# Kernel optimization log

Hardware: AMD Instinct MI355X
Metric: run time of the kernel (lower is better)

## Reference

```python
import jax, jax.numpy as jnp
import numpy as np
from jax import lax

B = 2
IMG = 640.0
MIN_LEVEL, MAX_LEVEL = 3, 7
NUM_CLASSES = 91          # includes background (index 0)
MAX_TOTAL = 100
IOU_THR = 0.3
SCORE_THR = 0.05
PRE_NMS = 5000
BBOX_CLIP = float(np.log(1000.0 / 16.0))  # standard box-transform clip


def _level_anchors(level):
    """RetinaNet-style anchors for one pyramid level, [H*W*9, 4] in (y1,x1,y2,x2)."""
    stride = 2 ** level
    feat = int(IMG) // stride
    cy = (np.arange(feat, dtype=np.float32) + 0.5) * stride
    cx = (np.arange(feat, dtype=np.float32) + 0.5) * stride
    cy, cx = np.meshgrid(cy, cx, indexing='ij')
    base = 4.0 * stride
    anchors = []
    for octave in (2 ** 0.0, 2 ** (1.0 / 3.0), 2 ** (2.0 / 3.0)):
        for ar in (0.5, 1.0, 2.0):
            h = base * octave * np.sqrt(ar)
            w = base * octave / np.sqrt(ar)
            anchors.append(np.stack([cy - h / 2, cx - w / 2, cy + h / 2, cx + w / 2], -1))
    a = np.stack(anchors, -2).reshape(-1, 4)
    return a.astype(np.float32)


def setup_inputs():
    key = jax.random.key(0)
    inp = {}
    for level in range(MIN_LEVEL, MAX_LEVEL + 1):
        anc = _level_anchors(level)
        n = anc.shape[0]
        key, kb, kc = jax.random.split(key, 3)
        inp[f'box_outputs_{level}'] = 0.2 * jax.random.normal(kb, (B, n, 4), jnp.float32)
        inp[f'class_outputs_{level}'] = jax.random.normal(kc, (B, n, NUM_CLASSES), jnp.float32) - 2.0
        inp[f'anchor_boxes_{level}'] = jnp.broadcast_to(jnp.asarray(anc)[None], (B, n, 4))
    inp['image_shape'] = jnp.full((B, 2), IMG, jnp.float32)
    return inp


def _decode_boxes(enc, anchors):
    # faithful to box_utils.decode_boxes (with the +1/-1 pixel convention)
    dy, dx = enc[..., 0], enc[..., 1]
    dh = jnp.minimum(enc[..., 2], BBOX_CLIP)
    dw = jnp.minimum(enc[..., 3], BBOX_CLIP)
    ah = anchors[..., 2] - anchors[..., 0] + 1.0
    aw = anchors[..., 3] - anchors[..., 1] + 1.0
    ayc = anchors[..., 0] + 0.5 * ah
    axc = anchors[..., 1] + 0.5 * aw
    yc = dy * ah + ayc
    xc = dx * aw + axc
    h = jnp.exp(dh) * ah
    w = jnp.exp(dw) * aw
    ymin = yc - 0.5 * h
    xmin = xc - 0.5 * w
    return jnp.stack([ymin, xmin, ymin + h - 1.0, xmin + w - 1.0], axis=-1)


def _clip_boxes(boxes, image_shape):
    h = image_shape[:, 0:1]
    w = image_shape[:, 1:2]
    max_len = jnp.stack([h, w, h, w], axis=-1)  # [B,1,4]
    return jnp.clip(boxes, 0.0, max_len)


def _greedy_nms(scores, boxes):
    """Sorted greedy NMS over one (batch, class) lane.
    scores: [K] sorted descending (filtered entries are -1), boxes: [K,4].
    Returns top MAX_TOTAL selected (score, box) in descending score order,
    padded with score=-1 / zero boxes (matches sorted_non_max_suppression_padded).
    """
    areas = (boxes[:, 2] - boxes[:, 0]) * (boxes[:, 3] - boxes[:, 1])

    def step(active, _):
        masked = jnp.where(active, scores, -jnp.inf)
        i = jnp.argmax(masked)
        s = masked[i]
        valid = s > -1.0
        b = boxes[i]
        yy1 = jnp.maximum(b[0], boxes[:, 0])
        xx1 = jnp.maximum(b[1], boxes[:, 1])
        yy2 = jnp.minimum(b[2], boxes[:, 2])
        xx2 = jnp.minimum(b[3], boxes[:, 3])
        inter = jnp.maximum(yy2 - yy1, 0.0) * jnp.maximum(xx2 - xx1, 0.0)
        iou = inter / ((b[2] - b[0]) * (b[3] - b[1]) + areas - inter + 1e-8)
        active = active & (iou <= IOU_THR)
        active = active.at[i].set(False)
        out_s = jnp.where(valid, s, -1.0)
        out_b = jnp.where(valid, b, jnp.zeros_like(b))
        return active, (out_s, out_b)

    _, (sel_s, sel_b) = lax.scan(step, jnp.ones(scores.shape[0], bool), None, length=MAX_TOTAL)
    return sel_s, sel_b


def reference(box_outputs_3, box_outputs_4, box_outputs_5, box_outputs_6, box_outputs_7,
              class_outputs_3, class_outputs_4, class_outputs_5, class_outputs_6, class_outputs_7,
              anchor_boxes_3, anchor_boxes_4, anchor_boxes_5, anchor_boxes_6, anchor_boxes_7,
              image_shape):
    box_list = [box_outputs_3, box_outputs_4, box_outputs_5, box_outputs_6, box_outputs_7]
    cls_list = [class_outputs_3, class_outputs_4, class_outputs_5, class_outputs_6, class_outputs_7]
    anc_list = [anchor_boxes_3, anchor_boxes_4, anchor_boxes_5, anchor_boxes_6, anchor_boxes_7]

    boxes, scores = [], []
    for bo, co, an in zip(box_list, cls_list, anc_list):
        scores.append(jax.nn.sigmoid(co)[..., 1:])            # drop background class 0
        boxes.append(_clip_boxes(_decode_boxes(bo, an), image_shape))
    boxes = jnp.concatenate(boxes, axis=1)                     # [B,N,4] class-agnostic
    scores = jnp.concatenate(scores, axis=1)                   # [B,N,C]

    scores_t = jnp.transpose(scores, (0, 2, 1))                # [B,C,N]
    k = min(scores_t.shape[-1], PRE_NMS)
    top_s, idx = lax.top_k(scores_t, k)                        # [B,C,K]
    top_b = jax.vmap(lambda b, i: b[i])(boxes, idx)            # [B,C,K,4]

    # filter_boxes_by_scores: score -> -1, boxes -> 0 below threshold
    mask = top_s >= SCORE_THR
    top_s = jnp.where(mask, top_s, -1.0)
    top_b = top_b * mask[..., None].astype(top_b.dtype)

    sel_s, sel_b = jax.vmap(jax.vmap(_greedy_nms))(top_s, top_b)  # [B,C,T], [B,C,T,4]
    Bsz, C, T = sel_s.shape
    classes = jnp.broadcast_to(jnp.arange(C, dtype=jnp.int32)[None, :, None], (Bsz, C, T))

    flat_s = sel_s.reshape(Bsz, C * T)
    flat_b = sel_b.reshape(Bsz, C * T, 4)
    flat_c = classes.reshape(Bsz, C * T)

    final_s, fidx = lax.top_k(flat_s, MAX_TOTAL)
    final_b = jnp.take_along_axis(flat_b, fidx[..., None], axis=1)
    final_c = jnp.take_along_axis(flat_c, fidx, axis=1) + 1    # nmsed_classes += 1
    valid = jnp.sum((final_s > -1.0).astype(jnp.int32), axis=1)
    return final_b, final_s, final_c, valid
```

## Files before the change

### kernel.cpp

```cpp
#include <hip/hip_runtime.h>
#include <hip/hip_bf16.h>

typedef unsigned long long u64;
typedef unsigned int u32;

#define A_TOTAL 76725
#define NCLS 90
#define KTOP 5000u
#define MAXT 100
#define KTHR 0x3D4CCCCDu
#define TCAP 2048u
#define SCAP 512u
#define BSTG 1024

__device__ __forceinline__ u64 pack_key(u32 k, u32 i) {
  return ((u64)k << 32) | (u64)(0xFFFFFFFFu - i);
}

__device__ __forceinline__ int dig05(u64 k) {
  float s = __uint_as_float((u32)(k >> 32));
  int d = (int)((s - 0.5f) * 8175.0f);
  return min(max(d, 0), 4095);
}

__device__ __forceinline__ void cut4096w(const u32* hh, u32 need, int wl,
                                         u32& B, u32& incl, u32& above, u32& total) {
  int lo = wl << 6;
  u32 s = 0;
  #pragma unroll
  for (int j = 0; j < 64; ++j) s += hh[lo + j];
  u32 suf = s;
  #pragma unroll
  for (int off = 1; off < 64; off <<= 1) {
    u32 v = __shfl_down(suf, off, 64);
    if (wl < 64 - off) suf += v;
  }
  total = __shfl(suf, 0, 64);
  if (total < need) { B = 0; incl = total; above = 0; return; }
  u32 sufnext = suf - s;
  bool cross = (suf >= need) && (sufnext < need);
  u64 bal = __ballot(cross);
  int gl = (int)__ffsll((unsigned long long)bal) - 1;
  int glo = gl << 6;
  u32 aboveG = __shfl(sufnext, gl, 64);
  u32 hb = hh[glo + wl];
  u32 sufb = hb;
  #pragma unroll
  for (int off = 1; off < 64; off <<= 1) {
    u32 v = __shfl_down(sufb, off, 64);
    if (wl < 64 - off) sufb += v;
  }
  bool c2 = (aboveG + sufb >= need) && (aboveG + sufb - hb < need);
  u64 bal2 = __ballot(c2);
  int jB = (int)__ffsll((unsigned long long)bal2) - 1;
  B = (u32)(glo + jB);
  incl = aboveG + __shfl(sufb, jB, 64);
  above = incl - __shfl(hb, jB, 64);
}

__device__ __forceinline__ void bitonic_desc(u64* a, u32 n, int tid, int nth) {
  u32 P = 2; while (P < n) P <<= 1;
  for (u32 i = tid; i < P; i += nth) if (i >= n) a[i] = 0ULL;
  __syncthreads();
  for (u32 kk = 2; kk <= P; kk <<= 1) {
    for (u32 jj = kk >> 1; jj; jj >>= 1) {
      for (u32 i = tid; i < P; i += nth) {
        u32 ixj = i ^ jj;
        if (ixj > i) {
          u64 x = a[i], y = a[ixj];
          bool up = ((i & kk) == 0);
          if (up ? (x < y) : (x > y)) { a[i] = y; a[ixj] = x; }
        }
      }
      __syncthreads();
    }
  }
}

__device__ __forceinline__ int lazy_scan_g(const u64* key_s, const float4* boxes4, size_t bbase,
                                           int C, float4* wbox, float* outS, float* outB,
                                           int w, int wl) {
  int cur = 0;
  while (w < MAXT && cur < C) {
    int p = cur + wl;
    bool alive = (p < C);
    u64 kk = alive ? key_s[p] : 0ull;
    float4 mybox = make_float4(0.f, 0.f, 0.f, 0.f);
    if (alive) {
      u32 idx = 0xFFFFFFFFu - (u32)(kk & 0xFFFFFFFFull);
      mybox = boxes4[bbase + idx];
    }
    float myarea = (mybox.z - mybox.x) * (mybox.w - mybox.y);
    for (int j = 0; j < w; ++j) {
      float4 pb = wbox[j];
      float yy1 = fmaxf(pb.x, mybox.x), xx1 = fmaxf(pb.y, mybox.y);
      float yy2 = fminf(pb.z, mybox.z), xx2 = fminf(pb.w, mybox.w);
      float inter = fmaxf(yy2 - yy1, 0.0f) * fmaxf(xx2 - xx1, 0.0f);
      bool bad = false;
      if (inter > 0.0f) {
        float pa = (pb.z - pb.x) * (pb.w - pb.y);
        bad = inter / (pa + myarea - inter + 1e-8f) > 0.3f;
      }
      alive = alive && !bad;
    }
    for (;;) {
      u64 bal = __ballot(alive);
      if (bal == 0ull) break;
      int js = (int)__ffsll((unsigned long long)bal) - 1;
      float4 pb;
      pb.x = __shfl(mybox.x, js, 64);
      pb.y = __shfl(mybox.y, js, 64);
      pb.z = __shfl(mybox.z, js, 64);
      pb.w = __shfl(mybox.w, js, 64);
      u64 wk = __shfl(kk, js, 64);
      if (wl == 0) {
        outS[w] = __uint_as_float((u32)(wk >> 32));
        *(float4*)(outB + w * 4) = pb;
        wbox[w] = pb;
      }
      w++;
      if (w >= MAXT) break;
      if (wl <= js) alive = false;
      else if (alive) {
        float yy1 = fmaxf(pb.x, mybox.x), xx1 = fmaxf(pb.y, mybox.y);
        float yy2 = fminf(pb.z, mybox.z), xx2 = fminf(pb.w, mybox.w);
        float inter = fmaxf(yy2 - yy1, 0.0f) * fmaxf(xx2 - xx1, 0.0f);
        if (inter > 0.0f) {
          float pa = (pb.z - pb.x) * (pb.w - pb.y);
          if (inter / (pa + myarea - inter + 1e-8f) > 0.3f) alive = false;
        }
      }
    }
    cur += 64;
  }
  return w;
}

__global__ __launch_bounds__(256) void zero_kernel(u32* __restrict__ p, int n) {
  int i = blockIdx.x * 256 + threadIdx.x;
  if (i < n) p[i] = 0;
}

__device__ __forceinline__ void coll_elem(int i, float x, int b, int base, int slice,
                                          u64* __restrict__ listT_g, u32* __restrict__ cnt_pad) {
  if (x >= 0.0f) {
    u32 a = (u32)i / 91u;
    u32 c = (u32)i - a * 91u;
    if (c != 0u) {
      float s = 1.0f / (1.0f + expf(-x));
      int lane = b * NCLS + (int)c - 1;
      u32 idx = (u32)base + a;
      u32 p = atomicAdd(&cnt_pad[lane * 128 + slice * 16], 1u);
      if (p < SCAP) listT_g[(((size_t)lane * 8 + slice) << 9) + p] = pack_key(__float_as_uint(s), idx);
    }
  }
}

__global__ __launch_bounds__(256) void front_kernel(
    const float* __restrict__ bx0, const float* __restrict__ bx1, const float* __restrict__ bx2,
    const float* __restrict__ bx3, const float* __restrict__ bx4,
    const float* __restrict__ an0, const float* __restrict__ an1, const float* __restrict__ an2,
    const float* __restrict__ an3, const float* __restrict__ an4,
    const float* __restrict__ c3, const float* __restrict__ c4, const float* __restrict__ c5,
    const float* __restrict__ c6, const float* __restrict__ c7,
    const float* __restrict__ img, float* __restrict__ boxes,
    u64* __restrict__ listT_g, u32* __restrict__ cnt_pad)
{
  int blk = blockIdx.x, tid = threadIdx.x;
  if (blk < 600) {
    int t = blk * 256 + tid;
    if (t >= 2 * A_TOTAL) return;
    int b = t / A_TOTAL, a = t % A_TOTAL;
    const float* bp; const float* ap; int al; int nl;
    if (a < 57600)      { bp = bx0; ap = an0; al = a;          nl = 57600; }
    else if (a < 72000) { bp = bx1; ap = an1; al = a - 57600;  nl = 14400; }
    else if (a < 75600) { bp = bx2; ap = an2; al = a - 72000;  nl = 3600;  }
    else if (a < 76500) { bp = bx3; ap = an3; al = a - 75600;  nl = 900;   }
    else                { bp = bx4; ap = an4; al = a - 76500;  nl = 225;   }
    float4 e  = *(const float4*)(bp + ((size_t)b * nl + al) * 4);
    float4 an = *(const float4*)(ap + ((size_t)b * nl + al) * 4);
    const float CLIP = 4.135166556742356f;
    float ah  = an.z - an.x + 1.0f;
    float aw  = an.w - an.y + 1.0f;
    float ayc = an.x + 0.5f * ah;
    float axc = an.y + 0.5f * aw;
    float dh = fminf(e.z, CLIP), dw = fminf(e.w, CLIP);
    float yc = e.x * ah + ayc;
    float xc = e.y * aw + axc;
    float h  = expf(dh) * ah;
    float w  = expf(dw) * aw;
    float ymin = yc - 0.5f * h;
    float xmin = xc - 0.5f * w;
    float ymax = ymin + h - 1.0f;
    float xmax = xmin + w - 1.0f;
    float H = img[b * 2 + 0], W = img[b * 2 + 1];
    float4 o;
    o.x = fminf(fmaxf(ymin, 0.0f), H);
    o.y = fminf(fmaxf(xmin, 0.0f), W);
    o.z = fminf(fmaxf(ymax, 0.0f), H);
    o.w = fminf(fmaxf(xmax, 0.0f), W);
    *(float4*)(boxes + (size_t)t * 4) = o;
    return;
  }
  int blk2 = blk - 600;
  int slice = blk2 & 7;
  const float* cls; int n, base, b, loc, J, lvl;
  if (blk2 < 2560)      { lvl = 0; cls = c3; n = 57600; base = 0;     J = 1280; int r = blk2;        b = r >= J; loc = b ? r - J : r; }
  else if (blk2 < 3200) { lvl = 1; cls = c4; n = 14400; base = 57600; J = 320;  int r = blk2 - 2560; b = r >= J; loc = b ? r - J : r; }
  else if (blk2 < 3360) { lvl = 2; cls = c5; n = 3600;  base = 72000; J = 80;   int r = blk2 - 3200; b = r >= J; loc = b ? r - J : r; }
  else if (blk2 < 3400) { lvl = 3; cls = c6; n = 900;   base = 75600; J = 20;   int r = blk2 - 3360; b = r >= J; loc = b ? r - J : r; }
  else                  { lvl = 4; cls = c7; n = 225;   base = 76500; J = 10;   int r = blk2 - 3400; b = r >= J; loc = b ? r - J : r; }

  if (lvl <= 3) {
    int F4 = n * 91 / 4;
    int chunk = (F4 + J - 1) / J;
    int q0 = loc * chunk;
    int q1 = q0 + chunk; if (q1 > F4) q1 = F4;
    const float4* src4 = (const float4*)(cls + (size_t)b * n * 91);
    for (int q = q0 + tid; q < q1; q += 256) {
      float4 v = src4[q];
      int i0 = q << 2;
      coll_elem(i0,     v.x, b, base, slice, listT_g, cnt_pad);
      coll_elem(i0 + 1, v.y, b, base, slice, listT_g, cnt_pad);
      coll_elem(i0 + 2, v.z, b, base, slice, listT_g, cnt_pad);
      coll_elem(i0 + 3, v.w, b, base, slice, listT_g, cnt_pad);
    }
  } else {
    int F = n * 91;
    int chunk = (F + J - 1) / J;
    int s0 = loc * chunk;
    int s1 = s0 + chunk; if (s1 > F) s1 = F;
    const float* src = cls + (size_t)b * F;
    for (int i = s0 + tid; i < s1; i += 256) coll_elem(i, src[i], b, base, slice, listT_g, cnt_pad);
  }
}

__global__ __launch_bounds__(256) void nms2_kernel(
    const u64* __restrict__ listT_g, const u32* __restrict__ cnt_pad,
    const float* __restrict__ boxes, u32* __restrict__ flags,
    float* __restrict__ nms_s, float* __restrict__ nms_b)
{
  __shared__ u32 histL[4096];
  __shared__ u64 key_s[2048];
  __shared__ float4 box_s[BSTG];
  __shared__ float4 wbox[MAXT];
  __shared__ u32 wtot[4];
  __shared__ u32 sh_big;
  int tid = threadIdx.x;
  int lane = blockIdx.x;

  u32 pre[9]; pre[0] = 0;
  bool of = false;
  #pragma unroll
  for (int j = 0; j < 8; ++j) {
    u32 cj = cnt_pad[lane * 128 + j * 16];
    of |= (cj > SCAP);
    pre[j + 1] = pre[j] + cj;
  }
  u32 cnt = pre[8];
  if (of || cnt > TCAP) {
    if (tid == 0) flags[lane] = 1;
    return;
  }
  if (tid == 0) sh_big = 0;

  u64 kr[8];
  #pragma unroll
  for (int r = 0; r < 8; ++r) {
    u32 s = (u32)tid + (u32)r * 256u;
    u64 k = 0ull;
    if (s < cnt) {
      u32 j = 0;
      #pragma unroll
      for (int t = 1; t < 8; ++t) if (s >= pre[t]) j = (u32)t;
      k = listT_g[(((size_t)lane * 8 + j) << 9) + (s - pre[j])];
    }
    kr[r] = k;
  }

  for (int i = tid; i < 4096; i += 256) histL[i] = 0;
  __syncthreads();
  #pragma unroll
  for (int r = 0; r < 8; ++r) if (kr[r]) atomicAdd(&histL[dig05(kr[r])], 1u);
  __syncthreads();
  {
    int t0 = tid << 4;
    u32 hloc[16]; u32 ssum = 0;
    #pragma unroll
    for (int j = 0; j < 16; ++j) { hloc[j] = histL[t0 + j]; ssum += hloc[j]; }
    int wl = tid & 63, wid = tid >> 6;
    u32 suf = ssum;
    #pragma unroll
    for (int off = 1; off < 64; off <<= 1) {
      u32 v = __shfl_down(suf, off, 64);
      if (wl < 64 - off) suf += v;
    }
    if (wl == 0) wtot[wid] = suf;
    __syncthreads();
    u32 cross = 0;
    for (int w2 = wid + 1; w2 < 4; ++w2) cross += wtot[w2];
    u32 run = (suf - ssum) + cross;
    #pragma unroll
    for (int j = 15; j >= 0; --j) { u32 b2 = run; run += hloc[j]; histL[t0 + j] = b2; }
  }
  __syncthreads();
  #pragma unroll
  for (int r = 0; r < 8; ++r) {
    u64 k = kr[r];
    if (k) {
      u32 pos = atomicAdd(&histL[dig05(k)], 1u);
      if (pos < TCAP) key_s[pos] = k;
    }
  }
  __syncthreads();
  {
    int t0 = tid << 4;
    for (int j = 0; j < 16; ++j) {
      u32 d = (u32)(t0 + j);
      u32 end = histL[d];
      u32 start = (d == 4095u) ? 0u : histL[d + 1];
      u32 cc = end - start;
      if (cc >= 2u) {
        if (cc <= 48u) {
          for (u32 a2 = start + 1; a2 < end; ++a2) {
            u64 kv = key_s[a2];
            int bi = (int)a2 - 1;
            while (bi >= (int)start && key_s[bi] < kv) { key_s[bi + 1] = key_s[bi]; --bi; }
            key_s[bi + 1] = kv;
          }
        } else sh_big = 1;
      }
    }
  }
  __syncthreads();
  if (sh_big) bitonic_desc(key_s, cnt, tid, 256);
  const float4* boxes4 = (const float4*)boxes;
  size_t bbase = (size_t)(lane / NCLS) * A_TOTAL;
  int C = (int)cnt;
  int nst = C < BSTG ? C : BSTG;
  for (int p = tid; p < nst; p += 256) {
    u32 idx = 0xFFFFFFFFu - (u32)(key_s[p] & 0xFFFFFFFFull);
    box_s[p] = boxes4[bbase + idx];
  }
  __syncthreads();
  if (tid >= 64) return;

  int wl = tid;
  float* outS = nms_s + (size_t)lane * MAXT;
  float* outB = nms_b + (size_t)lane * MAXT * 4;

  int w = 0, cur = 0;
  while (w < MAXT && cur < C) {
    int p = cur + wl;
    bool alive = (p < C);
    u64 kk = alive ? key_s[p] : 0ull;
    float4 mybox = make_float4(0.f, 0.f, 0.f, 0.f);
    if (alive) {
      if (p < BSTG) mybox = box_s[p];
      else {
        u32 idx = 0xFFFFFFFFu - (u32)(kk & 0xFFFFFFFFull);
        mybox = boxes4[bbase + idx];
      }
    }
    float myarea = (mybox.z - mybox.x) * (mybox.w - mybox.y);
    for (int j = 0; j < w; ++j) {
      float4 pb = wbox[j];
      float yy1 = fmaxf(pb.x, mybox.x), xx1 = fmaxf(pb.y, mybox.y);
      float yy2 = fminf(pb.z, mybox.z), xx2 = fminf(pb.w, mybox.w);
      float inter = fmaxf(yy2 - yy1, 0.0f) * fmaxf(xx2 - xx1, 0.0f);
      bool bad = false;
      if (inter > 0.0f) {
        float pa = (pb.z - pb.x) * (pb.w - pb.y);
        bad = inter / (pa + myarea - inter + 1e-8f) > 0.3f;
      }
      alive = alive && !bad;
    }
    for (;;) {
      u64 bal = __ballot(alive);
      if (bal == 0ull) break;
      int js = (int)__ffsll((unsigned long long)bal) - 1;
      int pw = cur + js;
      float4 pb;
      if (pw < BSTG) pb = box_s[pw];
      else {
        pb.x = __shfl(mybox.x, js, 64);
        pb.y = __shfl(mybox.y, js, 64);
        pb.z = __shfl(mybox.z, js, 64);
        pb.w = __shfl(mybox.w, js, 64);
      }
      if (wl == js) {
        wbox[w] = mybox;
        outS[w] = __uint_as_float((u32)(kk >> 32));
        *(float4*)(outB + w * 4) = mybox;
      }
      w++;
      if (w >= MAXT) break;
      if (wl <= js) alive = false;
      else if (alive) {
        float yy1 = fmaxf(pb.x, mybox.x), xx1 = fmaxf(pb.y, mybox.y);
        float yy2 = fminf(pb.z, mybox.z), xx2 = fminf(pb.w, mybox.w);
        float inter = fmaxf(yy2 - yy1, 0.0f) * fmaxf(xx2 - xx1, 0.0f);
        if (inter > 0.0f) {
          float pa = (pb.z - pb.x) * (pb.w - pb.y);
          if (inter / (pa + myarea - inter + 1e-8f) > 0.3f) alive = false;
        }
      }
    }
    cur += 64;
  }
  if (w < MAXT && wl == 0) flags[lane] = 1;
}

__global__ __launch_bounds__(256) void fb_kernel(
    const float* __restrict__ c3, const float* __restrict__ c4, const float* __restrict__ c5,
    const float* __restrict__ c6, const float* __restrict__ c7,
    const float* __restrict__ boxes, const u32* __restrict__ flags,
    float* __restrict__ nms_s, float* __restrict__ nms_b)
{
  __shared__ __align__(16) char big[40960];
  __shared__ __align__(16) u64 listE[2048];
  __shared__ u64 key_s[2048];
  __shared__ u32 histL[4096];
  __shared__ float4 wbox[MAXT];
  __shared__ u32 wtot[4];
  __shared__ u64 sh_minPrev;
  __shared__ u32 sh_w, sh_done, sh_eidx, sh_Rthr, sh_eSorted, sh_bigF;
  __shared__ u32 sh_B, sh_incl, sh_above, sh_total, sh_cA, sh_cE, sh_B2;

  int lane = blockIdx.x;
  if (flags[lane] == 0) return;
  int tid = threadIdx.x;
  int b = lane / NCLS, c = lane % NCLS;
  const float4* boxes4 = (const float4*)boxes;
  size_t bbase = (size_t)b * A_TOTAL;
  const u64 thrpack = ((u64)KTHR) << 32;

  float* outS = nms_s + (size_t)lane * MAXT;
  float* outB = nms_b + (size_t)lane * MAXT * 4;

  auto sb_of = [&](int i) -> u32 {
    const float* p; int al, nl;
    if (i < 57600)      { p = c3; al = i;          nl = 57600; }
    else if (i < 72000) { p = c4; al = i - 57600;  nl = 14400; }
    else if (i < 75600) { p = c5; al = i - 72000;  nl = 3600;  }
    else if (i < 76500) { p = c6; al = i - 75600;  nl = 900;   }
    else                { p = c7; al = i - 76500;  nl = 225;   }
    float x = p[((size_t)b * nl + al) * 91 + (c + 1)];
    float s = 1.0f / (1.0f + expf(-x));
    return __float_as_uint(s);
  };

  u64* listA = (u64*)big;
  for (int i = tid; i < 4096; i += 256) histL[i] = 0;
  if (tid == 0) {
    sh_cA = 0; sh_cE = 0; sh_w = 0; sh_done = 0; sh_eidx = 0; sh_eSorted = 0; sh_minPrev = ~0ull;
  }
  __syncthreads();
  for (int i = tid; i < A_TOTAL; i += 256) atomicAdd(&histL[sb_of(i) >> 19], 1u);
  __syncthreads();
  if (tid < 64) {
    u32 Bx, ix, ax, tx;
    cut4096w(histL, KTOP, tid, Bx, ix, ax, tx);
    if (tid == 0) sh_B = Bx;
  }
  __syncthreads();
  u32 B = sh_B;
  for (int i = tid; i < A_TOTAL; i += 256) {
    u32 u = sb_of(i);
    u32 bkt = u >> 19;
    if (bkt > B) {
      u32 p = atomicAdd(&sh_cA, 1u);
      if (p < 5120u) listA[p] = pack_key(u, (u32)i);
    } else if (bkt == B) {
      u32 p = atomicAdd(&sh_cE, 1u);
      if (p < 2048u) listE[p] = pack_key(u, (u32)i);
    }
  }
  __syncthreads();
  u32 g = sh_cA, h = sh_cE;
  if (h > 2048u) {
    for (int i = tid; i < 4096; i += 256) histL[i] = 0;
    if (tid == 0) sh_cE = 0;
    __syncthreads();
    for (int i = tid; i < A_TOTAL; i += 256) {
      u32 u = sb_of(i);
      if ((u >> 19) == B) atomicAdd(&histL[(u >> 7) & 0xFFFu], 1u);
    }
    __syncthreads();
    u32 R1 = KTOP - g;
    if (tid < 64) {
      u32 Bx, ix, ax, tx;
      cut4096w(histL, R1, tid, Bx, ix, ax, tx);
      if (tid == 0) sh_B2 = Bx;
    }
    __syncthreads();
    u32 B2 = sh_B2;
    for (int i = tid; i < A_TOTAL; i += 256) {
      u32 u = sb_of(i);
      if ((u >> 19) == B) {
        u32 sb2 = (u >> 7) & 0xFFFu;
        if (sb2 > B2) {
          u32 p = atomicAdd(&sh_cA, 1u);
          if (p < 5120u) listA[p] = pack_key(u, (u32)i);
        } else if (sb2 == B2) {
          u32 p = atomicAdd(&sh_cE, 1u);
          if (p < 2048u) listE[p] = pack_key(u, (u32)i);
        }
      }
    }
    __syncthreads();
    g = sh_cA; h = sh_cE; if (h > 2048u) h = 2048u;
  }
  if (g > 5120u) g = 5120u;
  u32 R = (g < KTOP) ? (KTOP - g) : 0u; if (R > h) R = h;

  u64 ak[20];
  #pragma unroll
  for (int r = 0; r < 20; ++r) {
    u32 s2 = (u32)tid + (u32)r * 256u;
    u64 kp = (s2 < g) ? listA[s2] : 0ull;
    if (kp < thrpack) kp = 0ull;
    ak[r] = kp;
  }
  __syncthreads();
  u32* cntArr = (u32*)big;

  const float LO0  = 0.04f;
  const float INV0 = 4096.0f / (1.001f - 0.04f);

  for (int seg = 0; seg < 7200; ++seg) {
    __syncthreads();
    if (sh_w >= MAXT || sh_done) break;
    u64 minPrev = sh_minPrev;

    int digLvl = 0;
    u32 A_B0 = 0, A_B1 = 0;
    float lo1 = 0.f, inv1 = 0.f;
    u64 kMask = 0, kPref = 0;
    int m1shift = 32;
    int selMode = -1;
    u32 selB = 0;
    u32 C = 0;
    bool fromE = false;

    for (int lvl = 0; lvl < 8; ++lvl) {
      for (int i = tid; i < 4096; i += 256) histL[i] = 0;
      __syncthreads();
      #pragma unroll
      for (int r = 0; r < 20; ++r) {
        u64 k = ak[r];
        if (!k || k >= minPrev) continue;
        float s = __uint_as_float((u32)(k >> 32));
        if (digLvl >= 1) { int d0 = (int)((s - LO0) * INV0); d0 = min(max(d0, 0), 4095); if ((u32)d0 != A_B0) continue; }
        if (digLvl >= 2) { int d1 = (int)((s - lo1) * inv1); d1 = min(max(d1, 0), 4095); if ((u32)d1 != A_B1) continue; }
        if (digLvl >= 3 && ((k & kMask) != kPref)) continue;
        u32 d;
        if (digLvl == 0)      { int t0 = (int)((s - LO0) * INV0); d = (u32)min(max(t0, 0), 4095); }
        else if (digLvl == 1) { int t1 = (int)((s - lo1) * inv1); d = (u32)min(max(t1, 0), 4095); }
        else                  d = (u32)((k >> m1shift) & 0xFFFull);
        atomicAdd(&histL[d], 1u);
      }
      __syncthreads();
      if (tid < 64) {
        u32 Bx, ix, ax, tx;
        cut4096w(histL, 1024u, tid, Bx, ix, ax, tx);
        if (tid == 0) { sh_B = Bx; sh_incl = ix; sh_above = ax; sh_total = tx; }
      }
      __syncthreads();
      u32 total = sh_total, incl = sh_incl, above = sh_above, Bx = sh_B;
      if (total == 0u)   { fromE = true; break; }
      if (total < 1024u) { selMode = 0; C = total; break; }
      if (incl <= 2048u) { selMode = 1; selB = Bx; C = incl; break; }
      if (above > 0u)    { selMode = 2; selB = Bx; C = above; break; }
      if (digLvl == 0) {
        A_B0 = Bx;
        lo1 = LO0 + (float)Bx / INV0;
        inv1 = INV0 * 4096.0f;
        digLvl = 1;
      } else if (digLvl == 1) {
        A_B1 = Bx;
        digLvl = 2; m1shift = 32;
      } else {
        kPref |= ((u64)Bx << m1shift);
        kMask |= (0xFFFull << m1shift);
        m1shift -= 12;
        digLvl++;
      }
      __syncthreads();
    }

    if (fromE) {
      if (!sh_eSorted) {
        bitonic_desc(listE, h, tid, 256);
        if (tid == 0) {
          u32 lo = 0, hi2 = h;
          while (lo < hi2) { u32 mid = (lo + hi2) >> 1; if (listE[mid] >= thrpack) lo = mid + 1; else hi2 = mid; }
          sh_Rthr = (R < lo) ? R : lo;
          sh_eSorted = 1;
        }
        __syncthreads();
      }
      u32 eidx = sh_eidx;
      u32 take = (sh_Rthr > eidx) ? (sh_Rthr - eidx) : 0u;
      if (take > 2048u) take = 2048u;
      if (take == 0u) { if (tid == 0) sh_done = 1; continue; }
      for (u32 i = tid; i < take; i += 256) key_s[i] = listE[eidx + i];
      C = take;
      if (tid == 0) sh_eidx = eidx + take;
    } else {
      u32 hloc[16];
      {
        int t0 = tid << 4;
        u32 ssum = 0;
        #pragma unroll
        for (int j = 0; j < 16; ++j) { hloc[j] = histL[t0 + j]; ssum += hloc[j]; }
        int wl = tid & 63, wid = tid >> 6;
        u32 suf = ssum;
        #pragma unroll
        for (int off = 1; off < 64; off <<= 1) {
          u32 v = __shfl_down(suf, off, 64);
          if (wl < 64 - off) suf += v;
        }
        if (wl == 0) wtot[wid] = suf;
        __syncthreads();
        u32 cross = 0;
        for (int w2 = wid + 1; w2 < 4; ++w2) cross += wtot[w2];
        u32 run = (suf - ssum) + cross;
        #pragma unroll
        for (int j = 15; j >= 0; --j) { u32 base2 = run; run += hloc[j]; histL[t0 + j] = base2; }
      }
      for (int i = tid; i < 4096; i += 256) cntArr[i] = 0;
      if (tid == 0) sh_bigF = 0;
      __syncthreads();
      #pragma unroll
      for (int r = 0; r < 20; ++r) {
        u64 k = ak[r];
        if (!k || k >= minPrev) continue;
        float s = __uint_as_float((u32)(k >> 32));
        if (digLvl >= 1) { int d0 = (int)((s - LO0) * INV0); d0 = min(max(d0, 0), 4095); if ((u32)d0 != A_B0) continue; }
        if (digLvl >= 2) { int d1 = (int)((s - lo1) * inv1); d1 = min(max(d1, 0), 4095); if ((u32)d1 != A_B1) continue; }
        if (digLvl >= 3 && ((k & kMask) != kPref)) continue;
        u32 d;
        if (digLvl == 0)      { int t0x = (int)((s - LO0) * INV0); d = (u32)min(max(t0x, 0), 4095); }
        else if (digLvl == 1) { int t1x = (int)((s - lo1) * inv1); d = (u32)min(max(t1x, 0), 4095); }
        else                  d = (u32)((k >> m1shift) & 0xFFFull);
        if (selMode == 1)      { if (d < selB) continue; }
        else if (selMode == 2) { if (d <= selB) continue; }
        u32 pos = histL[d] + atomicAdd(&cntArr[d], 1u);
        if (pos < 2048u) key_s[pos] = k;
      }
      __syncthreads();
      {
        int t0 = tid << 4;
        for (int j = 0; j < 16; ++j) {
          u32 bkt = (u32)(t0 + j);
          u32 cc = cntArr[bkt];
          if (cc >= 2u) {
            if (cc <= 48u) {
              u32 basep = histL[bkt];
              for (u32 a2 = 1; a2 < cc; ++a2) {
                u64 kv = key_s[basep + a2];
                int bi = (int)a2 - 1;
                while (bi >= 0 && key_s[basep + bi] < kv) { key_s[basep + bi + 1] = key_s[basep + bi]; --bi; }
                key_s[basep + bi + 1] = kv;
              }
            } else sh_bigF = 1;
          }
        }
      }
      __syncthreads();
      if (sh_bigF) bitonic_desc(key_s, C, tid, 256);
      if (tid == 0) sh_minPrev = key_s[C - 1];
    }
    __syncthreads();

    if (tid < 64) {
      int w = lazy_scan_g(key_s, boxes4, bbase, (int)C, wbox, outS, outB, (int)sh_w, tid);
      if (tid == 0) sh_w = (u32)w;
    }
  }

  __syncthreads();
  u32 w = sh_w;
  for (u32 p = w + (u32)tid; p < MAXT; p += 256) {
    outS[p] = -1.0f;
    *(float4*)(outB + p * 4) = make_float4(0.f, 0.f, 0.f, 0.f);
  }
}

__global__ __launch_bounds__(256) void merge_kernel(
    const float* __restrict__ nms_s, const float* __restrict__ nms_b,
    float* __restrict__ out_b, float* __restrict__ out_s,
    float* __restrict__ out_c, float* __restrict__ out_v)
{
  __shared__ u64 keys[NCLS * MAXT];
  __shared__ u32 hist[4096];
  __shared__ u64 sel[640];
  __shared__ u32 sh_cnt, sh_valid;
  __shared__ u32 sh_B, sh_incl, sh_above, sh_total;

  int b = blockIdx.x, tid = threadIdx.x;
  const int NTOT = NCLS * MAXT;

  for (int i = tid; i < NTOT; i += 256) {
    float s = nms_s[(size_t)b * NTOT + i];
    u32 u = __float_as_uint(s);
    u = (u & 0x80000000u) ? ~u : (u | 0x80000000u);
    keys[i] = ((u64)u << 32) | (u64)(0xFFFFFFFFu - (u32)i);
  }
  if (tid == 0) { sh_cnt = 0; sh_valid = 0; }

  u64 prefVal = 0;
  u64 T = 0;
  u32 need = MAXT;
  const int shifts[6] = {52, 40, 28, 16, 4, 0};
  const int widths[6] = {12, 12, 12, 12, 12, 4};
  for (int lvl = 0; lvl < 6; ++lvl) {
    int s = shifts[lvl], w = widths[lvl];
    for (int i = tid; i < 4096; i += 256) hist[i] = 0;
    __syncthreads();
    u32 dmask = (1u << w) - 1u;
    for (int i = tid; i < NTOT; i += 256) {
      u64 k = keys[i];
      if (lvl > 0 && (k >> (s + w)) != (prefVal >> (s + w))) continue;
      atomicAdd(&hist[(u32)((k >> s) & dmask)], 1u);
    }
    __syncthreads();
    if (tid < 64) {
      u32 Bx, ix, ax, tx;
      cut4096w(hist, need, tid, Bx, ix, ax, tx);
      if (tid == 0) { sh_B = Bx; sh_incl = ix; sh_above = ax; sh_total = tx; }
    }
    __syncthreads();
    u32 B = sh_B, incl = sh_incl, above = sh_above;
    if (incl <= 512u || lvl == 5) {
      T = prefVal | ((u64)B << s);
      break;
    }
    prefVal |= ((u64)B << s);
    need -= above;
  }
  __syncthreads();

  for (int i = tid; i < NTOT; i += 256) {
    u64 k = keys[i];
    if (k >= T) {
      u32 p = atomicAdd(&sh_cnt, 1u);
      if (p < 640u) sel[p] = k;
    }
  }
  __syncthreads();
  u32 cnt = sh_cnt; if (cnt > 640u) cnt = 640u;

  for (u32 j = tid; j < cnt; j += 256) {
    u64 kj = sel[j];
    u32 r = 0;
    for (u32 i = 0; i < cnt; ++i) r += (sel[i] > kj) ? 1u : 0u;
    if (r < (u32)MAXT) {
      u32 u = (u32)(kj >> 32);
      u32 bits = (u & 0x80000000u) ? (u ^ 0x80000000u) : ~u;
      float sc = __uint_as_float(bits);
      u32 flat = 0xFFFFFFFFu - (u32)(kj & 0xFFFFFFFFull);
      int cls = (int)(flat / MAXT), pos = (int)(flat % MAXT);
      out_s[b * MAXT + r] = sc;
      out_c[b * MAXT + r] = (float)(cls + 1);
      *(float4*)(out_b + ((size_t)b * MAXT + r) * 4) =
          *(const float4*)(nms_b + (((size_t)b * NCLS + cls) * MAXT + pos) * 4);
      if (sc > -1.0f) atomicAdd(&sh_valid, 1u);
    }
  }
  __syncthreads();
  if (tid == 0) out_v[b] = (float)sh_valid;
}

extern "C" void kernel_launch(void* const* d_in, const int* in_sizes, int n_in,
                              void* d_out, int out_size, void* d_ws, size_t ws_size,
                              hipStream_t stream)
{
  const float* box[5]; const float* cls[5]; const float* anc[5];
  bool interleaved = (in_sizes[1] == 2 * 57600 * 91);
  if (interleaved) {
    for (int l = 0; l < 5; ++l) {
      box[l] = (const float*)d_in[3 * l + 0];
      cls[l] = (const float*)d_in[3 * l + 1];
      anc[l] = (const float*)d_in[3 * l + 2];
    }
  } else {
    for (int l = 0; l < 5; ++l) {
      box[l] = (const float*)d_in[l];
      cls[l] = (const float*)d_in[5 + l];
      anc[l] = (const float*)d_in[10 + l];
    }
  }
  const float* img = (const float*)d_in[15];

  float* ws = (float*)d_ws;
  float* boxes_ws = ws;
  u32*   cnt_pad  = (u32*)(boxes_ws + 613800);
  u32*   flags    = cnt_pad + 180 * 128;
  u64*   listT_g  = (u64*)(flags + 180 + 4);
  float* nms_s    = (float*)(listT_g + 180 * 8 * 512);
  float* nms_b    = nms_s + 18000;

  const int NZ = 180 * 128 + 184;
  zero_kernel<<<(NZ + 255) / 256, 256, 0, stream>>>(cnt_pad, NZ);

  front_kernel<<<4020, 256, 0, stream>>>(
      box[0], box[1], box[2], box[3], box[4],
      anc[0], anc[1], anc[2], anc[3], anc[4],
      cls[0], cls[1], cls[2], cls[3], cls[4],
      img, boxes_ws, listT_g, cnt_pad);

  nms2_kernel<<<180, 256, 0, stream>>>(listT_g, cnt_pad, boxes_ws, flags, nms_s, nms_b);

  fb_kernel<<<180, 256, 0, stream>>>(cls[0], cls[1], cls[2], cls[3], cls[4],
                                     boxes_ws, flags, nms_s, nms_b);

  float* out_b = (float*)d_out;
  float* out_s = out_b + 800;
  float* out_c = out_s + 200;
  float* out_v = out_c + 200;
  merge_kernel<<<2, 256, 0, stream>>>(nms_s, nms_b, out_b, out_s, out_c, out_v);
}
```

Baseline: 125.7 us.

## Restructure NMS into 256-wide tiles with precomputed kill bitmask matrix

Replaces the single-wavefront sequential greedy NMS with a block-wide tiled scheme. All 256 threads load a tile of candidate boxes, test them against the already-kept boxes, then compute a 256x256 pairwise suppression bitmask in shared memory. One wavefront then resolves the greedy selection with bitwise operations on that mask. This spreads the IoU work across four wavefronts and drops the staged box_s cache, at the cost of computing the full pairwise matrix per tile and adding extra block barriers.

Measured after the change: 148.6 us. 1.18x slower.

```diff
diff --git a/kernel.cpp b/kernel.cpp
--- a/kernel.cpp
+++ b/kernel.cpp
@@ -11,7 +11,6 @@
 #define KTHR 0x3D4CCCCDu
 #define TCAP 2048u
 #define SCAP 512u
-#define BSTG 1024
 
 __device__ __forceinline__ u64 pack_key(u32 k, u32 i) {
   return ((u64)k << 32) | (u64)(0xFFFFFFFFu - i);
@@ -242,10 +241,13 @@
 {
   __shared__ u32 histL[4096];
   __shared__ u64 key_s[2048];
-  __shared__ float4 box_s[BSTG];
+  __shared__ float4 box_t[256];
+  __shared__ u32 Kmat[256 * 8];
   __shared__ float4 wbox[MAXT];
+  __shared__ u32 wlist[MAXT];
+  __shared__ u32 amask[8];
   __shared__ u32 wtot[4];
-  __shared__ u32 sh_big;
+  __shared__ u32 sh_big, sh_w;
   int tid = threadIdx.x;
   int lane = blockIdx.x;
 
@@ -262,7 +264,7 @@
     if (tid == 0) flags[lane] = 1;
     return;
   }
-  if (tid == 0) sh_big = 0;
+  if (tid == 0) { sh_big = 0; sh_w = 0; }
 
   u64 kr[8];
   #pragma unroll
@@ -334,36 +336,30 @@
   }
   __syncthreads();
   if (sh_big) bitonic_desc(key_s, cnt, tid, 256);
+
   const float4* boxes4 = (const float4*)boxes;
   size_t bbase = (size_t)(lane / NCLS) * A_TOTAL;
   int C = (int)cnt;
-  int nst = C < BSTG ? C : BSTG;
-  for (int p = tid; p < nst; p += 256) {
-    u32 idx = 0xFFFFFFFFu - (u32)(key_s[p] & 0xFFFFFFFFull);
-    box_s[p] = boxes4[bbase + idx];
-  }
-  __syncthreads();
-  if (tid >= 64) return;
-
-  int wl = tid;
+  int wq = tid >> 6, wl_ = tid & 63;
   float* outS = nms_s + (size_t)lane * MAXT;
   float* outB = nms_b + (size_t)lane * MAXT * 4;
 
-  int w = 0, cur = 0;
-  while (w < MAXT && cur < C) {
-    int p = cur + wl;
-    bool alive = (p < C);
-    u64 kk = alive ? key_s[p] : 0ull;
+  for (int t0 = 0; t0 < C; t0 += 256) {
+    __syncthreads();
+    int w0 = (int)sh_w;
+    if (w0 >= MAXT) break;
+    int p = t0 + tid;
+    bool valid = (p < C);
+    u64 kk = valid ? key_s[p] : 0ull;
     float4 mybox = make_float4(0.f, 0.f, 0.f, 0.f);
-    if (alive) {
-      if (p < BSTG) mybox = box_s[p];
-      else {
-        u32 idx = 0xFFFFFFFFu - (u32)(kk & 0xFFFFFFFFull);
-        mybox = boxes4[bbase + idx];
-      }
-    }
+    if (valid) {
+      u32 idx = 0xFFFFFFFFu - (u32)(kk & 0xFFFFFFFFull);
+      mybox = boxes4[bbase + idx];
+    }
+    box_t[tid] = mybox;
     float myarea = (mybox.z - mybox.x) * (mybox.w - mybox.y);
-    for (int j = 0; j < w; ++j) {
+    bool alive = valid;
+    for (int j = 0; j < w0; ++j) {
       float4 pb = wbox[j];
       float yy1 = fmaxf(pb.x, mybox.x), xx1 = fmaxf(pb.y, mybox.y);
       float yy2 = fminf(pb.z, mybox.z), xx2 = fminf(pb.w, mybox.w);
@@ -375,40 +371,64 @@
       }
       alive = alive && !bad;
     }
-    for (;;) {
-      u64 bal = __ballot(alive);
-      if (bal == 0ull) break;
-      int js = (int)__ffsll((unsigned long long)bal) - 1;
-      int pw = cur + js;
-      float4 pb;
-      if (pw < BSTG) pb = box_s[pw];
-      else {
-        pb.x = __shfl(mybox.x, js, 64);
-        pb.y = __shfl(mybox.y, js, 64);
-        pb.z = __shfl(mybox.z, js, 64);
-        pb.w = __shfl(mybox.w, js, 64);
-      }
-      if (wl == js) {
-        wbox[w] = mybox;
-        outS[w] = __uint_as_float((u32)(kk >> 32));
-        *(float4*)(outB + w * 4) = mybox;
-      }
-      w++;
-      if (w >= MAXT) break;
-      if (wl <= js) alive = false;
-      else if (alive) {
-        float yy1 = fmaxf(pb.x, mybox.x), xx1 = fmaxf(pb.y, mybox.y);
-        float yy2 = fminf(pb.z, mybox.z), xx2 = fminf(pb.w, mybox.w);
-        float inter = fmaxf(yy2 - yy1, 0.0f) * fmaxf(xx2 - xx1, 0.0f);
-        if (inter > 0.0f) {
-          float pa = (pb.z - pb.x) * (pb.w - pb.y);
-          if (inter / (pa + myarea - inter + 1e-8f) > 0.3f) alive = false;
+    __syncthreads();
+    u32 kw[8];
+    #pragma unroll
+    for (int l = 0; l < 8; ++l) kw[l] = 0;
+    int jmax = C - t0; if (jmax > 256) jmax = 256;
+    for (int j = 0; j < jmax; ++j) {
+      float4 pb = box_t[j];
+      float yy1 = fmaxf(pb.x, mybox.x), xx1 = fmaxf(pb.y, mybox.y);
+      float yy2 = fminf(pb.z, mybox.z), xx2 = fminf(pb.w, mybox.w);
+      float inter = fmaxf(yy2 - yy1, 0.0f) * fmaxf(xx2 - xx1, 0.0f);
+      bool kill = false;
+      if (inter > 0.0f) {
+        float pa = (pb.z - pb.x) * (pb.w - pb.y);
+        kill = inter / (pa + myarea - inter + 1e-8f) > 0.3f;
+      }
+      if (kill) kw[j >> 5] |= (1u << (j & 31));
+    }
+    #pragma unroll
+    for (int l = 0; l < 8; ++l) Kmat[tid * 8 + l] = kw[l];
+    u64 balA = __ballot(alive);
+    if (wl_ == 0) { amask[2 * wq] = (u32)balA; amask[2 * wq + 1] = (u32)(balA >> 32); }
+    __syncthreads();
+    if (tid < 64) {
+      u32 word = (tid < 8) ? amask[tid] : 0u;
+      int w = w0;
+      while (w < MAXT) {
+        u64 b2 = __ballot(word != 0u);
+        if (b2 == 0ull) break;
+        int lw = (int)__ffsll((unsigned long long)b2) - 1;
+        u32 wv = __shfl(word, lw, 64);
+        int bb = __ffs(wv) - 1;
+        int iw = (lw << 5) + bb;
+        if (tid == 0) wlist[w] = (u32)iw;
+        if (tid < 8) {
+          u32 krow = Kmat[iw * 8 + tid];
+          word &= ~krow;
+          if (tid == lw) word &= ~(1u << bb);
         }
-      }
-    }
-    cur += 64;
-  }
-  if (w < MAXT && wl == 0) flags[lane] = 1;
+        w++;
+      }
+      if (tid == 0) sh_w = (u32)w;
+    }
+    __syncthreads();
+    int w1 = (int)sh_w;
+    if (tid < w1 - w0) {
+      int wn = w0 + tid;
+      int iw = (int)wlist[wn];
+      u64 wk = key_s[t0 + iw];
+      float4 pb = box_t[iw];
+      outS[wn] = __uint_as_float((u32)(wk >> 32));
+      *(float4*)(outB + wn * 4) = pb;
+      wbox[wn] = pb;
+    }
+  }
+  __syncthreads();
+  if ((int)sh_w < MAXT) {
+    if (tid == 0) flags[lane] = 1;
+  }
 }
 
 __global__ __launch_bounds__(256) void fb_kernel(
```
